# Performance work log

Measured on AMD Instinct MI355X. Metric: run time of the kernel, lower is better.

The kernel has to match this reference:

```python
import jax, jax.numpy as jnp
import numpy as np

BLOCK = 128
E, T, H, I, K = 16, 512, 2048, 1408, 6

def _dequant(w, s):
    # w: (E, R, C), s: (E, R//BLOCK, C//BLOCK) block-wise inverse scales
    return w * jnp.repeat(jnp.repeat(s, BLOCK, axis=1), BLOCK, axis=2)

def setup_inputs() -> dict:
    key = jax.random.key(0)
    ks = jax.random.split(key, 9)
    return {
        "x": jax.random.normal(ks[0], (T, H), dtype=jnp.float32),
        "gate_weights": jax.random.normal(ks[1], (E, I, H), dtype=jnp.float32) * 0.05,
        "gate_scales": jax.random.uniform(ks[2], (E, I // BLOCK, H // BLOCK), dtype=jnp.float32),
        "up_weights": jax.random.normal(ks[3], (E, I, H), dtype=jnp.float32) * 0.05,
        "up_scales": jax.random.uniform(ks[4], (E, I // BLOCK, H // BLOCK), dtype=jnp.float32),
        "down_weights": jax.random.normal(ks[5], (E, H, I), dtype=jnp.float32) * 0.05,
        "down_scales": jax.random.uniform(ks[6], (E, H // BLOCK, I // BLOCK), dtype=jnp.float32),
        "routing_weights": jax.random.uniform(ks[7], (T, K), dtype=jnp.float32),
        "selected_experts": jax.random.randint(ks[8], (T, K), 0, E, dtype=jnp.int32),
    }

def reference(x, gate_weights, gate_scales, up_weights, up_scales,
              down_weights, down_scales, routing_weights, selected_experts):
    # Dequantize block-quantized expert weights
    wg = _dequant(gate_weights, gate_scales)   # (E, I, H)
    wu = _dequant(up_weights, up_scales)       # (E, I, H)
    wd = _dequant(down_weights, down_scales)   # (E, H, I)
    # Dense per-expert grouped GEMMs (reference path: all experts see all tokens)
    g = jnp.einsum('th,eih->eti', x, wg)       # (E, T, I)
    u = jnp.einsum('th,eih->eti', x, wu)
    h = jax.nn.silu(g) * u                     # SwiGLU
    y = jnp.einsum('eti,ehi->eth', h, wd)      # (E, T, H)
    # Combine: top-k routing weights scattered to (T, E) then contracted
    onehot = jax.nn.one_hot(selected_experts, E, dtype=x.dtype)  # (T, K, E)
    combine = jnp.einsum('tk,tke->et', routing_weights, onehot)  # (E, T)
    return jnp.einsum('et,eth->th', combine, y)                  # (T, H)
```

## Files before the change

### kernel.cpp

```cpp
#include <hip/hip_runtime.h>
#include <stdint.h>

#define E_NUM 16
#define T_TOK 512
#define H_DIM 2048
#define I_DIM 1408
#define K_TOP 6
#define CAP   512

#define TM  256
#define TN  32
#define BK  64
#define LDA 72

typedef __attribute__((ext_vector_type(8))) __bf16 bf16x8;
typedef __attribute__((ext_vector_type(4))) float f32x4;
typedef __attribute__((ext_vector_type(4))) unsigned short us4;
typedef __attribute__((ext_vector_type(8))) unsigned short us8;

__device__ __forceinline__ unsigned short f2bf(float f) {
  union { float f; unsigned u; } v; v.f = f;
  unsigned r = v.u + 0x7FFFu + ((v.u >> 16) & 1u);
  return (unsigned short)(r >> 16);
}

__global__ void k_routing(const float* __restrict__ rw, const int* __restrict__ sel,
                          int* counts, int* list, float* cw) {
  int t = blockIdx.x * blockDim.x + threadIdx.x;
  if (t >= T_TOK) return;
  int e[K_TOP]; float w[K_TOP];
#pragma unroll
  for (int k = 0; k < K_TOP; ++k) { e[k] = sel[t*K_TOP+k]; w[k] = rw[t*K_TOP+k]; }
#pragma unroll
  for (int k = 0; k < K_TOP; ++k) {
    bool dup = false;
#pragma unroll
    for (int j = 0; j < K_TOP; ++j) if (j < k && e[j] == e[k]) dup = true;
    if (!dup) {
      float c = 0.f;
#pragma unroll
      for (int j = 0; j < K_TOP; ++j) if (e[j] == e[k]) c += w[j];
      int slot = atomicAdd(&counts[e[k]], 1);
      list[e[k]*CAP + slot] = t;
      cw[e[k]*CAP + slot] = c;
    }
  }
}

__global__ void k_xcast(const float* __restrict__ x, unsigned short* __restrict__ xb) {
  int i = blockIdx.x * blockDim.x + threadIdx.x;
  const float4* src = (const float4*)x;
  float4 v0 = src[2*i], v1 = src[2*i+1];
  us8 o;
  o[0]=f2bf(v0.x); o[1]=f2bf(v0.y); o[2]=f2bf(v0.z); o[3]=f2bf(v0.w);
  o[4]=f2bf(v1.x); o[5]=f2bf(v1.y); o[6]=f2bf(v1.z); o[7]=f2bf(v1.w);
  *(us8*)(xb + (size_t)i*8) = o;
}

__global__ __launch_bounds__(256, 2)
void k_gateup(const unsigned short* __restrict__ xb,
              const float* __restrict__ Wg, const float* __restrict__ Sg,
              const float* __restrict__ Wu, const float* __restrict__ Su,
              const int* __restrict__ counts, const int* __restrict__ list,
              const float* __restrict__ cw, unsigned short* __restrict__ Hbuf) {
  __shared__ unsigned short sA[TM * LDA];
  __shared__ unsigned short sB[2 * TN * LDA];
  const int e   = blockIdx.y;
  const int n0  = blockIdx.x * TN;
  const int cnt = counts[e];
  if (cnt == 0) return;
  const int tid  = threadIdx.x;
  const int wv   = tid >> 6;
  const int lane = tid & 63;
  const int quad = lane >> 4;
  const int ln   = lane & 15;

  const int*   listE = list + e * CAP;
  const float* cwE   = cw + e * CAP;
  const float* WgE = Wg + (size_t)e * I_DIM * H_DIM + (size_t)n0 * H_DIM;
  const float* WuE = Wu + (size_t)e * I_DIM * H_DIM + (size_t)n0 * H_DIM;
  const float* SgE = Sg + e * (11*16) + (n0 >> 7) * 16;
  const float* SuE = Su + e * (11*16) + (n0 >> 7) * 16;
  unsigned short* HbE = Hbuf + (size_t)e * CAP * I_DIM;

  for (int m0 = 0; m0 < cnt; m0 += TM) {
    int tok[8];
#pragma unroll
    for (int j = 0; j < 8; ++j) {
      int m = m0 + j*32 + (tid >> 3);
      tok[j] = (m < cnt) ? listE[m] : listE[0];
    }
    f32x4 accG[4][2], accU[4][2];
#pragma unroll
    for (int mi = 0; mi < 4; ++mi)
#pragma unroll
      for (int ni = 0; ni < 2; ++ni) {
        accG[mi][ni] = (f32x4){0.f,0.f,0.f,0.f};
        accU[mi][ni] = (f32x4){0.f,0.f,0.f,0.f};
      }

    for (int kc = 0; kc < H_DIM / BK; ++kc) {
      const int k0 = kc * BK;
      __syncthreads();
      const int seg = tid & 7;
#pragma unroll
      for (int j = 0; j < 8; ++j) {
        int row = j*32 + (tid >> 3);
        uint4 v = *(const uint4*)(xb + (size_t)tok[j]*H_DIM + k0 + seg*8);
        *(uint4*)(sA + row*LDA + seg*8) = v;
      }
      const float sG = SgE[k0 >> 7];
      const float sU = SuE[k0 >> 7];
#pragma unroll
      for (int j = 0; j < 4; ++j) {
        int p = j*256 + tid;
        int mat = p >> 9;
        int row = (p >> 4) & 31;
        int sg4 = p & 15;
        const float* W = (mat ? WuE : WgE) + (size_t)row * H_DIM + k0 + sg4*4;
        float s = mat ? sU : sG;
        float4 v = *(const float4*)W;
        us4 o;
        o.x = f2bf(v.x * s); o.y = f2bf(v.y * s);
        o.z = f2bf(v.z * s); o.w = f2bf(v.w * s);
        *(us4*)(sB + (mat*TN + row)*LDA + sg4*4) = o;
      }
      __syncthreads();
#pragma unroll
      for (int ks = 0; ks < 2; ++ks) {
        bf16x8 a[4], bg[2], bu[2];
#pragma unroll
        for (int mi = 0; mi < 4; ++mi)
          a[mi] = *(const bf16x8*)(sA + (wv*64 + mi*16 + ln)*LDA + ks*32 + quad*8);
#pragma unroll
        for (int ni = 0; ni < 2; ++ni) {
          bg[ni] = *(const bf16x8*)(sB + (ni*16 + ln)*LDA + ks*32 + quad*8);
          bu[ni] = *(const bf16x8*)(sB + (TN + ni*16 + ln)*LDA + ks*32 + quad*8);
        }
#pragma unroll
        for (int mi = 0; mi < 4; ++mi)
#pragma unroll
          for (int ni = 0; ni < 2; ++ni) {
            accG[mi][ni] = __builtin_amdgcn_mfma_f32_16x16x32_bf16(a[mi], bg[ni], accG[mi][ni], 0, 0, 0);
            accU[mi][ni] = __builtin_amdgcn_mfma_f32_16x16x32_bf16(a[mi], bu[ni], accU[mi][ni], 0, 0, 0);
          }
      }
    }
#pragma unroll
    for (int mi = 0; mi < 4; ++mi)
#pragma unroll
      for (int r = 0; r < 4; ++r) {
        int m = m0 + wv*64 + mi*16 + quad*4 + r;
        if (m < cnt) {
          float c = cwE[m];
#pragma unroll
          for (int ni = 0; ni < 2; ++ni) {
            float g = accG[mi][ni][r];
            float u = accU[mi][ni][r];
            float h = g / (1.f + __expf(-g)) * u * c;
            HbE[(size_t)m * I_DIM + n0 + ni*16 + ln] = f2bf(h);
          }
        }
      }
  }
}

__global__ __launch_bounds__(256, 2)
void k_down(const unsigned short* __restrict__ Hbuf,
            const float* __restrict__ Wd, const float* __restrict__ Sd,
            const int* __restrict__ counts, const int* __restrict__ list,
            float* __restrict__ out) {
  __shared__ unsigned short sA[TM * LDA];
  __shared__ unsigned short sB[TN * LDA];
  const int e   = blockIdx.y;
  const int n0  = blockIdx.x * TN;
  const int cnt = counts[e];
  if (cnt == 0) return;
  const int tid  = threadIdx.x;
  const int wv   = tid >> 6;
  const int lane = tid & 63;
  const int quad = lane >> 4;
  const int ln   = lane & 15;

  const int* listE = list + e * CAP;
  const unsigned short* HbE = Hbuf + (size_t)e * CAP * I_DIM;
  const float* WdE = Wd + (size_t)e * H_DIM * I_DIM + (size_t)n0 * I_DIM;
  const float* SdE = Sd + e * (16*11) + (n0 >> 7) * 11;

  for (int m0 = 0; m0 < cnt; m0 += TM) {
    f32x4 acc[4][2];
#pragma unroll
    for (int mi = 0; mi < 4; ++mi)
#pragma unroll
      for (int ni = 0; ni < 2; ++ni)
        acc[mi][ni] = (f32x4){0.f,0.f,0.f,0.f};

    for (int kc = 0; kc < I_DIM / BK; ++kc) {
      const int k0 = kc * BK;
      __syncthreads();
      const int seg = tid & 7;
#pragma unroll
      for (int j = 0; j < 8; ++j) {
        int row = j*32 + (tid >> 3);
        uint4 v = *(const uint4*)(HbE + (size_t)(m0 + row)*I_DIM + k0 + seg*8);
        *(uint4*)(sA + row*LDA + seg*8) = v;
      }
      const float s = SdE[k0 >> 7];
#pragma unroll
      for (int j = 0; j < 2; ++j) {
        int p = j*256 + tid;
        int row = p >> 4;
        int sg4 = p & 15;
        float4 v = *(const float4*)(WdE + (size_t)row * I_DIM + k0 + sg4*4);
        us4 o;
        o.x = f2bf(v.x * s); o.y = f2bf(v.y * s);
        o.z = f2bf(v.z * s); o.w = f2bf(v.w * s);
        *(us4*)(sB + row*LDA + sg4*4) = o;
      }
      __syncthreads();
#pragma unroll
      for (int ks = 0; ks < 2; ++ks) {
        bf16x8 a[4], b[2];
#pragma unroll
        for (int mi = 0; mi < 4; ++mi)
          a[mi] = *(const bf16x8*)(sA + (wv*64 + mi*16 + ln)*LDA + ks*32 + quad*8);
#pragma unroll
        for (int ni = 0; ni < 2; ++ni)
          b[ni] = *(const bf16x8*)(sB + (ni*16 + ln)*LDA + ks*32 + quad*8);
#pragma unroll
        for (int mi = 0; mi < 4; ++mi)
#pragma unroll
          for (int ni = 0; ni < 2; ++ni)
            acc[mi][ni] = __builtin_amdgcn_mfma_f32_16x16x32_bf16(a[mi], b[ni], acc[mi][ni], 0, 0, 0);
      }
    }
#pragma unroll
    for (int mi = 0; mi < 4; ++mi)
#pragma unroll
      for (int r = 0; r < 4; ++r) {
        int m = m0 + wv*64 + mi*16 + quad*4 + r;
        if (m < cnt) {
          int t = listE[m];
#pragma unroll
          for (int ni = 0; ni < 2; ++ni)
            atomicAdd(out + (size_t)t * H_DIM + n0 + ni*16 + ln, acc[mi][ni][r]);
        }
      }
  }
}

extern "C" void kernel_launch(void* const* d_in, const int* in_sizes, int n_in,
                              void* d_out, int out_size, void* d_ws, size_t ws_size,
                              hipStream_t stream) {
  const float* x  = (const float*)d_in[0];
  const float* Wg = (const float*)d_in[1];
  const float* Sg = (const float*)d_in[2];
  const float* Wu = (const float*)d_in[3];
  const float* Su = (const float*)d_in[4];
  const float* Wd = (const float*)d_in[5];
  const float* Sd = (const float*)d_in[6];
  const float* rw = (const float*)d_in[7];
  const int*  sel = (const int*)d_in[8];
  float* out = (float*)d_out;

  char* ws = (char*)d_ws;
  int*   counts = (int*)ws;
  int*   list   = (int*)(ws + 256);
  float* cw     = (float*)(ws + 256 + 32768);
  unsigned short* xb   = (unsigned short*)(ws + 256 + 65536);
  unsigned short* Hbuf = (unsigned short*)(ws + 256 + 65536 + (size_t)T_TOK*H_DIM*2);
  (void)in_sizes; (void)n_in; (void)out_size; (void)ws_size;

  hipMemsetAsync(counts, 0, 256, stream);
  hipMemsetAsync(out, 0, sizeof(float) * (size_t)T_TOK * H_DIM, stream);
  k_routing<<<dim3((T_TOK + 255) / 256), dim3(256), 0, stream>>>(rw, sel, counts, list, cw);
  k_xcast<<<dim3((T_TOK * H_DIM) / 2048), dim3(256), 0, stream>>>(x, xb);
  k_gateup<<<dim3(I_DIM / TN, E_NUM), dim3(256), 0, stream>>>(xb, Wg, Sg, Wu, Su, counts, list, cw, Hbuf);
  k_down<<<dim3(H_DIM / TN, E_NUM), dim3(256), 0, stream>>>(Hbuf, Wd, Sd, counts, list, out);
}
```

Baseline: 669.0 us.

## Prefetch next K-tile into registers during MFMA compute in both GEMM kernels

Both gate/up and down kernels now issue global loads for the next K chunk into registers right after the LDS barrier, so memory latency overlaps the MFMA loop. Staging to LDS then comes from those registers. Launch bounds also rise from 2 to 3 blocks per SM, which tightens the register budget while the prefetch buffers add register pressure. This risks spills, and the last iteration makes a redundant wrapped load.

```diff
diff --git a/kernel.cpp b/kernel.cpp
--- a/kernel.cpp
+++ b/kernel.cpp
@@ -57,7 +57,7 @@
   *(us8*)(xb + (size_t)i*8) = o;
 }
 
-__global__ __launch_bounds__(256, 2)
+__global__ __launch_bounds__(256, 3)
 void k_gateup(const unsigned short* __restrict__ xb,
               const float* __restrict__ Wg, const float* __restrict__ Sg,
               const float* __restrict__ Wu, const float* __restrict__ Su,
@@ -74,6 +74,10 @@
   const int lane = tid & 63;
   const int quad = lane >> 4;
   const int ln   = lane & 15;
+  const int seg  = tid & 7;
+  const int arow = tid >> 3;
+  const int bmatHalf = tid >> 9;
+  (void)bmatHalf;
 
   const int*   listE = list + e * CAP;
   const float* cwE   = cw + e * CAP;
@@ -83,11 +87,13 @@
   const float* SuE = Su + e * (11*16) + (n0 >> 7) * 16;
   unsigned short* HbE = Hbuf + (size_t)e * CAP * I_DIM;
 
+  const int NKC = H_DIM / BK;
+
   for (int m0 = 0; m0 < cnt; m0 += TM) {
     int tok[8];
 #pragma unroll
     for (int j = 0; j < 8; ++j) {
-      int m = m0 + j*32 + (tid >> 3);
+      int m = m0 + j*32 + arow;
       tok[j] = (m < cnt) ? listE[m] : listE[0];
     }
     f32x4 accG[4][2], accU[4][2];
@@ -99,33 +105,48 @@
         accU[mi][ni] = (f32x4){0.f,0.f,0.f,0.f};
       }
 
-    for (int kc = 0; kc < H_DIM / BK; ++kc) {
+    uint4  Areg[8];
+    float4 Breg[4];
+#pragma unroll
+    for (int j = 0; j < 8; ++j)
+      Areg[j] = *(const uint4*)(xb + (size_t)tok[j]*H_DIM + seg*8);
+#pragma unroll
+    for (int j = 0; j < 4; ++j) {
+      int p = j*256 + tid;
+      int mat = p >> 9, row = (p >> 4) & 31, sg4 = p & 15;
+      Breg[j] = *(const float4*)((mat ? WuE : WgE) + (size_t)row * H_DIM + sg4*4);
+    }
+
+    for (int kc = 0; kc < NKC; ++kc) {
       const int k0 = kc * BK;
       __syncthreads();
-      const int seg = tid & 7;
-#pragma unroll
-      for (int j = 0; j < 8; ++j) {
-        int row = j*32 + (tid >> 3);
-        uint4 v = *(const uint4*)(xb + (size_t)tok[j]*H_DIM + k0 + seg*8);
-        *(uint4*)(sA + row*LDA + seg*8) = v;
-      }
+#pragma unroll
+      for (int j = 0; j < 8; ++j)
+        *(uint4*)(sA + (j*32 + arow)*LDA + seg*8) = Areg[j];
       const float sG = SgE[k0 >> 7];
       const float sU = SuE[k0 >> 7];
 #pragma unroll
       for (int j = 0; j < 4; ++j) {
         int p = j*256 + tid;
-        int mat = p >> 9;
-        int row = (p >> 4) & 31;
-        int sg4 = p & 15;
-        const float* W = (mat ? WuE : WgE) + (size_t)row * H_DIM + k0 + sg4*4;
+        int mat = p >> 9, row = (p >> 4) & 31, sg4 = p & 15;
         float s = mat ? sU : sG;
-        float4 v = *(const float4*)W;
+        float4 v = Breg[j];
         us4 o;
         o.x = f2bf(v.x * s); o.y = f2bf(v.y * s);
         o.z = f2bf(v.z * s); o.w = f2bf(v.w * s);
         *(us4*)(sB + (mat*TN + row)*LDA + sg4*4) = o;
       }
       __syncthreads();
+      const int kn = (kc + 1 < NKC) ? k0 + BK : 0;
+#pragma unroll
+      for (int j = 0; j < 8; ++j)
+        Areg[j] = *(const uint4*)(xb + (size_t)tok[j]*H_DIM + kn + seg*8);
+#pragma unroll
+      for (int j = 0; j < 4; ++j) {
+        int p = j*256 + tid;
+        int mat = p >> 9, row = (p >> 4) & 31, sg4 = p & 15;
+        Breg[j] = *(const float4*)((mat ? WuE : WgE) + (size_t)row * H_DIM + kn + sg4*4);
+      }
 #pragma unroll
       for (int ks = 0; ks < 2; ++ks) {
         bf16x8 a[4], bg[2], bu[2];
@@ -165,7 +186,7 @@
   }
 }
 
-__global__ __launch_bounds__(256, 2)
+__global__ __launch_bounds__(256, 3)
 void k_down(const unsigned short* __restrict__ Hbuf,
             const float* __restrict__ Wd, const float* __restrict__ Sd,
             const int* __restrict__ counts, const int* __restrict__ list,
@@ -181,12 +202,16 @@
   const int lane = tid & 63;
   const int quad = lane >> 4;
   const int ln   = lane & 15;
+  const int seg  = tid & 7;
+  const int arow = tid >> 3;
 
   const int* listE = list + e * CAP;
   const unsigned short* HbE = Hbuf + (size_t)e * CAP * I_DIM;
   const float* WdE = Wd + (size_t)e * H_DIM * I_DIM + (size_t)n0 * I_DIM;
   const float* SdE = Sd + e * (16*11) + (n0 >> 7) * 11;
 
+  const int NKC = I_DIM / BK;
+
   for (int m0 = 0; m0 < cnt; m0 += TM) {
     f32x4 acc[4][2];
 #pragma unroll
@@ -195,29 +220,46 @@
       for (int ni = 0; ni < 2; ++ni)
         acc[mi][ni] = (f32x4){0.f,0.f,0.f,0.f};
 
-    for (int kc = 0; kc < I_DIM / BK; ++kc) {
+    uint4  Areg[8];
+    float4 Breg[2];
+#pragma unroll
+    for (int j = 0; j < 8; ++j)
+      Areg[j] = *(const uint4*)(HbE + (size_t)(m0 + j*32 + arow)*I_DIM + seg*8);
+#pragma unroll
+    for (int j = 0; j < 2; ++j) {
+      int p = j*256 + tid;
+      int row = p >> 4, sg4 = p & 15;
+      Breg[j] = *(const float4*)(WdE + (size_t)row * I_DIM + sg4*4);
+    }
+
+    for (int kc = 0; kc < NKC; ++kc) {
       const int k0 = kc * BK;
       __syncthreads();
-      const int seg = tid & 7;
-#pragma unroll
-      for (int j = 0; j < 8; ++j) {
-        int row = j*32 + (tid >> 3);
-        uint4 v = *(const uint4*)(HbE + (size_t)(m0 + row)*I_DIM + k0 + seg*8);
-        *(uint4*)(sA + row*LDA + seg*8) = v;
-      }
+#pragma unroll
+      for (int j = 0; j < 8; ++j)
+        *(uint4*)(sA + (j*32 + arow)*LDA + seg*8) = Areg[j];
       const float s = SdE[k0 >> 7];
 #pragma unroll
       for (int j = 0; j < 2; ++j) {
         int p = j*256 + tid;
-        int row = p >> 4;
-        int sg4 = p & 15;
-        float4 v = *(const float4*)(WdE + (size_t)row * I_DIM + k0 + sg4*4);
+        int row = p >> 4, sg4 = p & 15;
+        float4 v = Breg[j];
         us4 o;
         o.x = f2bf(v.x * s); o.y = f2bf(v.y * s);
         o.z = f2bf(v.z * s); o.w = f2bf(v.w * s);
         *(us4*)(sB + row*LDA + sg4*4) = o;
       }
       __syncthreads();
+      const int kn = (kc + 1 < NKC) ? k0 + BK : 0;
+#pragma unroll
+      for (int j = 0; j < 8; ++j)
+        Areg[j] = *(const uint4*)(HbE + (size_t)(m0 + j*32 + arow)*I_DIM + kn + seg*8);
+#pragma unroll
+      for (int j = 0; j < 2; ++j) {
+        int p = j*256 + tid;
+        int row = p >> 4, sg4 = p & 15;
+        Breg[j] = *(const float4*)(WdE + (size_t)row * I_DIM + kn + sg4*4);
+      }
 #pragma unroll
       for (int ks = 0; ks < 2; ++ks) {
         bf16x8 a[4], b[2];
```

Measured after the change: 967.2 us. 1.45x slower.
